# Kernel tuning notes

Hardware: AMD Instinct MI355X
Metric: run time of the kernel (lower is better)

Reference implementation:

```python
import jax, jax.numpy as jnp
import numpy as np
import math

HEAD_DIM = 64
N_Q = 64
N_KV = 8
HIDDEN = 2880
SLIDING = 128
BASE = 150000.0
INIT_CTX = 4096
SCALE = 32.0
NTK_A = 1.0
NTK_B = 32.0
SEQ = 2048


def _rope_cos_sin(position_ids):
    # YaRN-scaled inverse frequencies (scaling_factor > 1 branch)
    freq = BASE ** (jnp.arange(0, HEAD_DIM, 2, dtype=jnp.float32) / HEAD_DIM)
    concentration = 0.1 * math.log(SCALE) + 1.0
    d_half = HEAD_DIM // 2
    low = d_half * math.log(INIT_CTX / (NTK_B * 2 * math.pi)) / math.log(BASE)
    high = d_half * math.log(INIT_CTX / (NTK_A * 2 * math.pi)) / math.log(BASE)
    interpolation = 1.0 / (SCALE * freq)
    extrapolation = 1.0 / freq
    ramp = (jnp.arange(d_half, dtype=jnp.float32) - low) / (high - low)
    mask = 1.0 - jnp.clip(ramp, 0.0, 1.0)
    inv_freq = interpolation * (1.0 - mask) + extrapolation * mask
    freqs = position_ids.astype(jnp.float32)[:, None] * inv_freq[None, :]  # [n, d/2]
    return jnp.cos(freqs) * concentration, jnp.sin(freqs) * concentration


def _apply_rope(x, cos, sin):
    # x: [n, h, d]; cos/sin: [n, d/2]
    cos = cos[:, None, :].astype(x.dtype)
    sin = sin[:, None, :].astype(x.dtype)
    x1, x2 = jnp.split(x, 2, axis=-1)
    return jnp.concatenate([x1 * cos - x2 * sin, x2 * cos + x1 * sin], axis=-1)


def setup_inputs() -> dict:
    key = jax.random.key(0)
    ks = jax.random.split(key, 6)
    qkv_dim = HEAD_DIM * (N_Q + 2 * N_KV)
    return {
        "hidden_states": jax.random.normal(ks[0], (SEQ, HIDDEN), dtype=jnp.float32),
        "qkv_w": jax.random.normal(ks[1], (qkv_dim, HIDDEN), dtype=jnp.float32) * 0.02,
        "qkv_b": jax.random.normal(ks[2], (qkv_dim,), dtype=jnp.float32) * 0.02,
        "o_w": jax.random.normal(ks[3], (HIDDEN, N_Q * HEAD_DIM), dtype=jnp.float32) * 0.02,
        "o_b": jax.random.normal(ks[4], (HIDDEN,), dtype=jnp.float32) * 0.02,
        "sinks": jax.random.normal(ks[5], (N_Q,), dtype=jnp.float32),
        "position_ids": jnp.arange(SEQ, dtype=jnp.int64 if jax.config.jax_enable_x64 else jnp.int32),
    }


def reference(hidden_states, qkv_w, qkv_b, o_w, o_b, sinks, position_ids):
    n = hidden_states.shape[0]
    scaling = HEAD_DIM ** (-0.5)

    # fused QKV projection + split
    qkv = hidden_states @ qkv_w.T + qkv_b  # [n, (nq+2*nkv)*d]
    q_sz, k_sz = N_Q * HEAD_DIM, N_KV * HEAD_DIM
    q = qkv[:, :q_sz].reshape(n, N_Q, HEAD_DIM)
    k = qkv[:, q_sz:q_sz + k_sz].reshape(n, N_KV, HEAD_DIM)
    v = qkv[:, q_sz + k_sz:].reshape(n, N_KV, HEAD_DIM)

    # RoPE (YaRN)
    cos, sin = _rope_cos_sin(position_ids)
    q = _apply_rope(q, cos, sin)
    k = _apply_rope(k, cos, sin)

    # GQA: repeat KV heads to match query heads
    groups = N_Q // N_KV
    k_full = jnp.repeat(k, groups, axis=1)  # [n, N_Q, d]
    v_full = jnp.repeat(v, groups, axis=1)

    scores = jnp.einsum('qhd,khd->hqk', q, k_full) * scaling  # [H, S, S]

    # sliding-window mask (distance > window -> -inf), as in source (no causal term)
    current_pos = position_ids.max()
    key_pos = current_pos - n + 1 + jnp.arange(n)
    dist = position_ids[:, None] - key_pos[None, :]
    win_mask = jnp.where(dist > SLIDING, -jnp.inf, 0.0).astype(scores.dtype)
    scores = scores + win_mask[None, :, :]

    # learned sink logit appended to softmax normalization
    sink = jnp.broadcast_to(sinks[:, None, None], (N_Q, n, 1)).astype(scores.dtype)
    logits = jnp.concatenate([scores, sink], axis=-1)  # [H, S, S+1]
    probs = jax.nn.softmax(logits, axis=-1)[..., :-1]   # drop sink column

    attn = jnp.einsum('hqk,khd->qhd', probs, v_full)    # [S, H, d]
    attn = attn.reshape(n, N_Q * HEAD_DIM)
    return attn @ o_w.T + o_b
```

## Files before the change

kernel.cpp:

```cpp
#include <hip/hip_runtime.h>
#include <hip/hip_bf16.h>
#include <stdint.h>

typedef __attribute__((ext_vector_type(4))) float f32x4;
typedef __attribute__((ext_vector_type(8))) short bf16x8;

#define SEQ 2048
#define HIDDEN 2880
#define NQ 64
#define NKV 8
#define HD 64
#define QKV_DIM 5120
#define Q_SZ 4096
#define K_SZ 512
#define OW_N 2880
#define OW_NPAD 2944
#define OW_K 4096

__device__ __forceinline__ unsigned short f2b_bits(float f) {
    unsigned int x = __float_as_uint(f);
    unsigned int r = (x + 0x7fffu + ((x >> 16) & 1u)) >> 16;
    return (unsigned short)r;
}
__device__ __forceinline__ float b2f(unsigned short u) {
    return __uint_as_float(((unsigned int)u) << 16);
}

__device__ __forceinline__ void llds16(const ushort* g, ushort* l) {
    __builtin_amdgcn_global_load_lds(
        (const __attribute__((address_space(1))) void*)g,
        (__attribute__((address_space(3))) void*)l, 16, 0, 0);
}

__global__ void convert_all(const float* __restrict__ hidden, const float* __restrict__ qkv_w,
                            const float* __restrict__ o_w, ushort* __restrict__ hs_bf,
                            ushort* __restrict__ wqkv_bf, ushort* __restrict__ wo_bf) {
    const int N1 = SEQ * HIDDEN / 4;
    const int N2 = N1 + QKV_DIM * HIDDEN / 4;
    const int N3 = N2 + OW_NPAD * OW_K / 4;
    int i = blockIdx.x * blockDim.x + threadIdx.x;
    int stride = gridDim.x * blockDim.x;
    for (; i < N3; i += stride) {
        const float* src;
        ushort* dst;
        int j;
        if (i < N1) {
            j = i; src = hidden; dst = hs_bf;
        } else if (i < N2) {
            j = i - N1; src = qkv_w; dst = wqkv_bf;
        } else {
            j = i - N2; src = o_w; dst = wo_bf;
            if ((j >> 10) >= OW_N) {
                reinterpret_cast<ushort4*>(dst)[j] = make_ushort4(0, 0, 0, 0);
                continue;
            }
        }
        float4 v = reinterpret_cast<const float4*>(src)[j];
        reinterpret_cast<ushort4*>(dst)[j] =
            make_ushort4(f2b_bits(v.x), f2b_bits(v.y), f2b_bits(v.z), f2b_bits(v.w));
    }
}

template<int OUT_BF16>
__global__ __launch_bounds__(256) void gemm_bt(
    const ushort* __restrict__ A, const ushort* __restrict__ B,
    const float* __restrict__ bias, void* __restrict__ Cout,
    int M, int N, int K, int Nreal, int ldC)
{
    __shared__ __align__(16) ushort As[128 * 64];
    __shared__ __align__(16) ushort Bs[128 * 64];
    const int tid = threadIdx.x;
    const int lane = tid & 63;
    const int w = tid >> 6;
    const int wr = w >> 1, wc = w & 1;

    const int nwg = gridDim.x;
    const int per = nwg >> 3;
    const int wgid = (blockIdx.x & 7) * per + (blockIdx.x >> 3);
    const int m0 = (wgid & 15) * 128;
    const int n0 = (wgid >> 4) * 128;

    f32x4 acc[4][4] = {};

    for (int k0 = 0; k0 < K; k0 += 64) {
        #pragma unroll
        for (int it = 0; it < 4; ++it) {
            int i = it * 256 + tid;
            int row = i >> 3;
            int col16 = (i ^ (row & 7)) & 7;
            llds16(A + (size_t)(m0 + row) * K + k0 + col16 * 8,
                   As + (size_t)(it * 256 + (tid & ~63)) * 8);
            llds16(B + (size_t)(n0 + row) * K + k0 + col16 * 8,
                   Bs + (size_t)(it * 256 + (tid & ~63)) * 8);
        }
        __syncthreads();
        #pragma unroll
        for (int kk = 0; kk < 2; ++kk) {
            bf16x8 a[4], b[4];
            #pragma unroll
            for (int mi = 0; mi < 4; ++mi) {
                int row = wr * 64 + mi * 16 + (lane & 15);
                int byte = row * 128 + kk * 64 + (lane >> 4) * 16;
                byte ^= (row & 7) << 4;
                a[mi] = *reinterpret_cast<const bf16x8*>(reinterpret_cast<const char*>(As) + byte);
            }
            #pragma unroll
            for (int ni = 0; ni < 4; ++ni) {
                int row = wc * 64 + ni * 16 + (lane & 15);
                int byte = row * 128 + kk * 64 + (lane >> 4) * 16;
                byte ^= (row & 7) << 4;
                b[ni] = *reinterpret_cast<const bf16x8*>(reinterpret_cast<const char*>(Bs) + byte);
            }
            #pragma unroll
            for (int mi = 0; mi < 4; ++mi)
                #pragma unroll
                for (int ni = 0; ni < 4; ++ni)
                    acc[mi][ni] = __builtin_amdgcn_mfma_f32_16x16x32_bf16(a[mi], b[ni], acc[mi][ni], 0, 0, 0);
        }
        __syncthreads();
    }

    #pragma unroll
    for (int mi = 0; mi < 4; ++mi) {
        int gr = m0 + wr * 64 + mi * 16 + (lane >> 4) * 4;
        #pragma unroll
        for (int ni = 0; ni < 4; ++ni) {
            int gc = n0 + wc * 64 + ni * 16 + (lane & 15);
            if (gc < Nreal) {
                float bv = bias[gc];
                #pragma unroll
                for (int r = 0; r < 4; ++r) {
                    float v = acc[mi][ni][r] + bv;
                    if (OUT_BF16)
                        ((ushort*)Cout)[(size_t)(gr + r) * ldC + gc] = f2b_bits(v);
                    else
                        ((float*)Cout)[(size_t)(gr + r) * ldC + gc] = v;
                }
            }
        }
    }
}

template<int OUT_BF16>
__global__ __launch_bounds__(256) void gemm_bt64(
    const ushort* __restrict__ A, const ushort* __restrict__ B,
    const float* __restrict__ bias, void* __restrict__ Cout,
    int M, int N, int K, int Nreal, int ldC)
{
    __shared__ __align__(16) ushort As[64 * 64];
    __shared__ __align__(16) ushort Bs[128 * 64];
    const int tid = threadIdx.x;
    const int lane = tid & 63;
    const int w = tid >> 6;
    const int l15 = lane & 15;
    const int l4 = lane >> 4;

    const int nwg = gridDim.x;
    const int per = nwg >> 3;
    const int wgid = (blockIdx.x & 7) * per + (blockIdx.x >> 3);
    const int m0 = (wgid & 31) * 64;
    const int n0 = (wgid >> 5) * 128;

    f32x4 acc[4][2] = {};

    for (int k0 = 0; k0 < K; k0 += 64) {
        #pragma unroll
        for (int it = 0; it < 2; ++it) {
            int i = it * 256 + tid;
            int row = i >> 3;
            int col16 = (i ^ (row & 7)) & 7;
            llds16(A + (size_t)(m0 + row) * K + k0 + col16 * 8,
                   As + (size_t)(it * 256 + (tid & ~63)) * 8);
        }
        #pragma unroll
        for (int it = 0; it < 4; ++it) {
            int i = it * 256 + tid;
            int row = i >> 3;
            int col16 = (i ^ (row & 7)) & 7;
            llds16(B + (size_t)(n0 + row) * K + k0 + col16 * 8,
                   Bs + (size_t)(it * 256 + (tid & ~63)) * 8);
        }
        __syncthreads();
        #pragma unroll
        for (int kk = 0; kk < 2; ++kk) {
            bf16x8 a[4], b[2];
            #pragma unroll
            for (int mi = 0; mi < 4; ++mi) {
                int row = mi * 16 + l15;
                int byte = row * 128 + kk * 64 + l4 * 16;
                byte ^= (row & 7) << 4;
                a[mi] = *reinterpret_cast<const bf16x8*>(reinterpret_cast<const char*>(As) + byte);
            }
            #pragma unroll
            for (int ni = 0; ni < 2; ++ni) {
                int row = w * 32 + ni * 16 + l15;
                int byte = row * 128 + kk * 64 + l4 * 16;
                byte ^= (row & 7) << 4;
                b[ni] = *reinterpret_cast<const bf16x8*>(reinterpret_cast<const char*>(Bs) + byte);
            }
            #pragma unroll
            for (int mi = 0; mi < 4; ++mi)
                #pragma unroll
                for (int ni = 0; ni < 2; ++ni)
                    acc[mi][ni] = __builtin_amdgcn_mfma_f32_16x16x32_bf16(a[mi], b[ni], acc[mi][ni], 0, 0, 0);
        }
        __syncthreads();
    }

    #pragma unroll
    for (int mi = 0; mi < 4; ++mi) {
        int gr = m0 + mi * 16 + l4 * 4;
        #pragma unroll
        for (int ni = 0; ni < 2; ++ni) {
            int gc = n0 + w * 32 + ni * 16 + l15;
            if (gc < Nreal) {
                float bv = bias[gc];
                #pragma unroll
                for (int r = 0; r < 4; ++r) {
                    float v = acc[mi][ni][r] + bv;
                    if (OUT_BF16)
                        ((ushort*)Cout)[(size_t)(gr + r) * ldC + gc] = f2b_bits(v);
                    else
                        ((float*)Cout)[(size_t)(gr + r) * ldC + gc] = v;
                }
            }
        }
    }
}

__global__ __launch_bounds__(256) void rope_kernel(
    const ushort* __restrict__ qkv, const int* __restrict__ pos,
    ushort* __restrict__ q_ro, ushort* __restrict__ k_ro)
{
    __shared__ float cosv[32], sinv[32];
    const int s = blockIdx.x;
    const int tid = threadIdx.x;
    if (tid < 32) {
        int j = tid;
        const float logbase = logf(150000.0f);
        float freq = expf((float)j * (logbase / 32.0f));
        float interp = 1.0f / (32.0f * freq);
        float extrap = 1.0f / freq;
        const float twopi = 6.283185307179586f;
        float low  = 32.0f * logf(4096.0f / (32.0f * twopi)) / logbase;
        float high = 32.0f * logf(4096.0f / (1.0f  * twopi)) / logbase;
        float ramp = ((float)j - low) / (high - low);
        float mask = 1.0f - fminf(fmaxf(ramp, 0.0f), 1.0f);
        float inv_freq = interp * (1.0f - mask) + extrap * mask;
        float ang = (float)pos[s] * inv_freq;
        const float conc = 0.1f * logf(32.0f) + 1.0f;
        cosv[j] = cosf(ang) * conc;
        sinv[j] = sinf(ang) * conc;
    }
    __syncthreads();
    const float qsc = 0.125f * 1.4426950408889634f;
    #pragma unroll
    for (int it = 0; it < 8; ++it) {
        int idx = it * 256 + tid;
        int h = idx >> 5, j = idx & 31;
        const ushort* src = qkv + (size_t)s * QKV_DIM + h * HD;
        float x1 = b2f(src[j]), x2 = b2f(src[j + 32]);
        float c = cosv[j], sn = sinv[j];
        ushort* dst = q_ro + ((size_t)h * SEQ + s) * HD;
        dst[j]      = f2b_bits((x1 * c - x2 * sn) * qsc);
        dst[j + 32] = f2b_bits((x2 * c + x1 * sn) * qsc);
    }
    {
        int h = tid >> 5, j = tid & 31;
        const ushort* src = qkv + (size_t)s * QKV_DIM + Q_SZ + h * HD;
        float x1 = b2f(src[j]), x2 = b2f(src[j + 32]);
        float c = cosv[j], sn = sinv[j];
        ushort* dst = k_ro + ((size_t)h * SEQ + s) * HD;
        dst[j]      = f2b_bits(x1 * c - x2 * sn);
        dst[j + 32] = f2b_bits(x2 * c + x1 * sn);
    }
}

__global__ __launch_bounds__(256) void vtrans_kernel(const ushort* __restrict__ qkv, ushort* __restrict__ vT) {
    __shared__ ushort t[64][65];
    const int kh = blockIdx.x >> 5;
    const int s0 = (blockIdx.x & 31) * 64;
    const int tid = threadIdx.x;
    #pragma unroll
    for (int it = 0; it < 16; ++it) {
        int e = it * 256 + tid;
        int sl = e >> 6, d = e & 63;
        t[d][sl] = qkv[(size_t)(s0 + sl) * QKV_DIM + Q_SZ + K_SZ + kh * HD + d];
    }
    __syncthreads();
    #pragma unroll
    for (int it = 0; it < 16; ++it) {
        int e = it * 256 + tid;
        int d = e >> 6, sl = e & 63;
        vT[((size_t)kh * HD + d) * SEQ + s0 + sl] = t[d][sl];
    }
}

__global__ __launch_bounds__(256, 4) void attn_kernel(
    const ushort* __restrict__ q_ro, const ushort* __restrict__ k_ro,
    const ushort* __restrict__ vT, const float* __restrict__ sinks,
    ushort* __restrict__ attn_out)
{
    __shared__ __align__(16) ushort Kb[2][4096];
    __shared__ __align__(16) ushort Vb[2][4096];

    const int tid = threadIdx.x;
    const int lane = tid & 63;
    const int w = tid >> 6;
    const int l15 = lane & 15;
    const int l4 = lane >> 4;

    int wg = blockIdx.x;
    int wgid = (wg & 7) * 128 + (wg >> 3);
    const int kh = wgid >> 7;
    const int qh = (wgid >> 4) & 7;
    const int pp = wgid & 15;
    const int h = kh * 8 + qh;

    const float snk = sinks[h];

    const short oneb = (short)0x3F80;
    const bf16x8 bones = {oneb, oneb, oneb, oneb, oneb, oneb, oneb, oneb};

    const int i0 = tid, i1 = 256 + tid;
    const int r0 = i0 >> 3, cs0 = (i0 ^ r0) & 7;
    const int r1 = i1 >> 3, cs1 = (i1 ^ r1) & 7;
    const ushort* gK0 = k_ro + (size_t)kh * (SEQ * 64) + r0 * 64 + cs0 * 8;
    const ushort* gK1 = k_ro + (size_t)kh * (SEQ * 64) + r1 * 64 + cs1 * 8;
    const ushort* gV0 = vT + ((size_t)kh * 64 + r0) * SEQ + cs0 * 8;
    const ushort* gV1 = vT + ((size_t)kh * 64 + r1) * SEQ + cs1 * 8;
    const int ld0 = (tid & ~63) * 8, ld1 = (256 + (tid & ~63)) * 8;

    const int swz = (l15 & 7) << 4;
    const int kvbase = l15 * 128 + ((l4 * 16) ^ swz);
    const int pwbase = l15 * 128 + ((l4 * 8) ^ swz);

    auto stage = [&](int bs, int k0) {
        llds16(gK0 + k0 * 64, &Kb[bs][ld0]);
        llds16(gK1 + k0 * 64, &Kb[bs][ld1]);
        llds16(gV0 + k0,      &Vb[bs][ld0]);
        llds16(gV1 + k0,      &Vb[bs][ld1]);
    };

    for (int sidx = 0; sidx < 2; ++sidx) {
        const int qt = sidx ? (31 - pp) : pp;
        const int q0 = qt * 64;
        const int qw = q0 + w * 16;

        bf16x8 aq[2];
        #pragma unroll
        for (int kc = 0; kc < 2; ++kc)
            aq[kc] = *reinterpret_cast<const bf16x8*>(
                q_ro + ((size_t)h * SEQ + qw + l15) * HD + kc * 32 + l4 * 8);

        f32x4 o[4] = {};
        f32x4 lacc = {0.f, 0.f, 0.f, 0.f};

        const int kt0 = (qt >= 2) ? (qt - 2) : 0;
        int cur = 0;

        stage(0, kt0 * 64);
        __syncthreads();

        for (int kt = kt0; kt < SEQ / 64; ++kt) {
            const int k0 = kt * 64;
            if (kt + 1 < SEQ / 64) stage(cur ^ 1, k0 + 64);

            f32x4 s[4];
            const f32x4 z = {0.f, 0.f, 0.f, 0.f};
            const char* kbp = (const char*)Kb[cur];
            __builtin_amdgcn_s_setprio(1);
            #pragma unroll
            for (int c = 0; c < 4; ++c) {
                bf16x8 bk0 = *reinterpret_cast<const bf16x8*>(kbp + c * 2048 + kvbase);
                s[c] = __builtin_amdgcn_mfma_f32_16x16x32_bf16(bk0, aq[0], z, 0, 0, 0);
                bf16x8 bk1 = *reinterpret_cast<const bf16x8*>(kbp + c * 2048 + (kvbase ^ 64));
                s[c] = __builtin_amdgcn_mfma_f32_16x16x32_bf16(bk1, aq[1], s[c], 0, 0, 0);
            }
            __builtin_amdgcn_s_setprio(0);

            if (k0 < qw - 113) {
                int thr = qw + l15 - 128 - k0;
                #pragma unroll
                for (int c = 0; c < 4; ++c)
                    #pragma unroll
                    for (int r = 0; r < 4; ++r)
                        if (c * 16 + l4 * 4 + r < thr) s[c][r] = -1e30f;
            }

            __builtin_amdgcn_s_barrier();
            char* pw = (char*)Kb[cur] + w * 2048;

            #pragma unroll
            for (int c = 0; c < 4; ++c) {
                float p0 = exp2f(s[c][0]), p1 = exp2f(s[c][1]);
                float p2 = exp2f(s[c][2]), p3 = exp2f(s[c][3]);
                unsigned int pk0, pk1;
                asm("v_cvt_pk_bf16_f32 %0, %1, %2" : "=v"(pk0) : "v"(p0), "v"(p1));
                asm("v_cvt_pk_bf16_f32 %0, %1, %2" : "=v"(pk1) : "v"(p2), "v"(p3));
                uint2 pv; pv.x = pk0; pv.y = pk1;
                *reinterpret_cast<uint2*>(pw + (pwbase ^ (c * 32))) = pv;
            }

            const char* vbp = (const char*)Vb[cur];
            __builtin_amdgcn_s_setprio(1);
            #pragma unroll
            for (int kc = 0; kc < 2; ++kc) {
                bf16x8 pa = *reinterpret_cast<const bf16x8*>(pw + (kvbase ^ (kc * 64)));
                lacc = __builtin_amdgcn_mfma_f32_16x16x32_bf16(pa, bones, lacc, 0, 0, 0);
                #pragma unroll
                for (int df = 0; df < 4; ++df) {
                    bf16x8 bv = *reinterpret_cast<const bf16x8*>(vbp + df * 2048 + (kvbase ^ (kc * 64)));
                    o[df] = __builtin_amdgcn_mfma_f32_16x16x32_bf16(pa, bv, o[df], 0, 0, 0);
                }
            }
            __builtin_amdgcn_s_setprio(0);

            __syncthreads();
            cur ^= 1;
        }

        {
            const float es = exp2f(snk * 1.4426950408889634f);
            float inv[4];
            #pragma unroll
            for (int r = 0; r < 4; ++r) inv[r] = 1.0f / (lacc[r] + es);
            #pragma unroll
            for (int df = 0; df < 4; ++df)
                #pragma unroll
                for (int r = 0; r < 4; ++r) {
                    int row = qw + l4 * 4 + r;
                    int col = df * 16 + l15;
                    attn_out[(size_t)row * Q_SZ + h * HD + col] = f2b_bits(o[df][r] * inv[r]);
                }
        }
    }
}

extern "C" void kernel_launch(void* const* d_in, const int* in_sizes, int n_in,
                              void* d_out, int out_size, void* d_ws, size_t ws_size,
                              hipStream_t stream) {
    const float* hidden = (const float*)d_in[0];
    const float* qkv_w  = (const float*)d_in[1];
    const float* qkv_b  = (const float*)d_in[2];
    const float* o_w    = (const float*)d_in[3];
    const float* o_b    = (const float*)d_in[4];
    const float* sinks  = (const float*)d_in[5];
    const int*   pos    = (const int*)d_in[6];
    float* out = (float*)d_out;

    char* ws = (char*)d_ws;
    size_t off = 0;
    auto alloc = [&](size_t bytes) {
        char* p = ws + off;
        off += (bytes + 255) & ~(size_t)255;
        return p;
    };
    ushort* hs_bf   = (ushort*)alloc((size_t)SEQ * HIDDEN * 2);
    ushort* wqkv_bf = (ushort*)alloc((size_t)QKV_DIM * HIDDEN * 2);
    ushort* qkv_bf  = (ushort*)alloc((size_t)SEQ * QKV_DIM * 2);
    ushort* q_ro    = (ushort*)alloc((size_t)NQ * SEQ * HD * 2);
    ushort* k_ro    = (ushort*)alloc((size_t)NKV * SEQ * HD * 2);
    ushort* vT      = (ushort*)alloc((size_t)NKV * HD * SEQ * 2);
    ushort* attn_bf = (ushort*)alloc((size_t)SEQ * Q_SZ * 2);
    ushort* wo_bf   = (ushort*)alloc((size_t)OW_NPAD * OW_K * 2);

    convert_all<<<2048, 256, 0, stream>>>(hidden, qkv_w, o_w, hs_bf, wqkv_bf, wo_bf);

    gemm_bt<1><<<(QKV_DIM / 128) * (SEQ / 128), 256, 0, stream>>>(
        hs_bf, wqkv_bf, qkv_b, qkv_bf, SEQ, QKV_DIM, HIDDEN, QKV_DIM, QKV_DIM);

    rope_kernel<<<SEQ, 256, 0, stream>>>(qkv_bf, pos, q_ro, k_ro);
    vtrans_kernel<<<NKV * 32, 256, 0, stream>>>(qkv_bf, vT);

    attn_kernel<<<1024, 256, 0, stream>>>(q_ro, k_ro, vT, sinks, attn_bf);

    gemm_bt64<0><<<(OW_NPAD / 128) * (SEQ / 64), 256, 0, stream>>>(
        attn_bf, wo_bf, o_b, out, SEQ, OW_NPAD, OW_K, OW_N, OW_N);
}
```

Baseline: 262.0 us.

## Process both query strips in one KV sweep with a dedicated P buffer

Each workgroup used to handle its two query tiles (pp and 31-pp) one after the other, loading the K/V stream twice. Now a single pass over the KV tiles serves both, so strip B reuses the already staged K/V tiles once its window starts. The probability tile moves from the K buffer into a separate per-wave LDS array, which removes the extra barrier before the P write. The cost is more accumulator registers (two sets of o, lacc and q fragments) and more LDS per block, which may lower occupancy at launch bounds of 4.

```diff
diff --git a/kernel.cpp b/kernel.cpp
--- a/kernel.cpp
+++ b/kernel.cpp
@@ -303,6 +303,7 @@
 {
     __shared__ __align__(16) ushort Kb[2][4096];
     __shared__ __align__(16) ushort Vb[2][4096];
+    __shared__ __align__(16) ushort Pl[4][1024];
 
     const int tid = threadIdx.x;
     const int lane = tid & 63;
@@ -318,6 +319,7 @@
     const int h = kh * 8 + qh;
 
     const float snk = sinks[h];
+    char* pbase = (char*)&Pl[w][0];
 
     const short oneb = (short)0x3F80;
     const bf16x8 bones = {oneb, oneb, oneb, oneb, oneb, oneb, oneb, oneb};
@@ -342,98 +344,108 @@
         llds16(gV1 + k0,      &Vb[bs][ld1]);
     };
 
-    for (int sidx = 0; sidx < 2; ++sidx) {
-        const int qt = sidx ? (31 - pp) : pp;
-        const int q0 = qt * 64;
-        const int qw = q0 + w * 16;
-
-        bf16x8 aq[2];
-        #pragma unroll
-        for (int kc = 0; kc < 2; ++kc)
-            aq[kc] = *reinterpret_cast<const bf16x8*>(
-                q_ro + ((size_t)h * SEQ + qw + l15) * HD + kc * 32 + l4 * 8);
-
-        f32x4 o[4] = {};
-        f32x4 lacc = {0.f, 0.f, 0.f, 0.f};
-
-        const int kt0 = (qt >= 2) ? (qt - 2) : 0;
-        int cur = 0;
-
-        stage(0, kt0 * 64);
+    const int qtA = pp;
+    const int qtB = 31 - pp;
+    const int qwA = qtA * 64 + w * 16;
+    const int qwB = qtB * 64 + w * 16;
+    const int ktA0 = (qtA >= 2) ? (qtA - 2) : 0;
+    const int ktB0 = qtB - 2;
+
+    bf16x8 aqA[2], aqB[2];
+    #pragma unroll
+    for (int kc = 0; kc < 2; ++kc) {
+        aqA[kc] = *reinterpret_cast<const bf16x8*>(
+            q_ro + ((size_t)h * SEQ + qwA + l15) * HD + kc * 32 + l4 * 8);
+        aqB[kc] = *reinterpret_cast<const bf16x8*>(
+            q_ro + ((size_t)h * SEQ + qwB + l15) * HD + kc * 32 + l4 * 8);
+    }
+
+    f32x4 oA[4] = {}, oB[4] = {};
+    f32x4 laccA = {0.f, 0.f, 0.f, 0.f}, laccB = {0.f, 0.f, 0.f, 0.f};
+
+    int cur = 0;
+    stage(0, ktA0 * 64);
+    __syncthreads();
+
+    auto strip_body = [&](const bf16x8 (&aq)[2], f32x4 (&o)[4], f32x4& lacc,
+                          int qw, int k0, const char* kbp, const char* vbp) {
+        f32x4 s[4];
+        const f32x4 z = {0.f, 0.f, 0.f, 0.f};
+        __builtin_amdgcn_s_setprio(1);
+        #pragma unroll
+        for (int c = 0; c < 4; ++c) {
+            bf16x8 bk0 = *reinterpret_cast<const bf16x8*>(kbp + c * 2048 + kvbase);
+            s[c] = __builtin_amdgcn_mfma_f32_16x16x32_bf16(bk0, aq[0], z, 0, 0, 0);
+            bf16x8 bk1 = *reinterpret_cast<const bf16x8*>(kbp + c * 2048 + (kvbase ^ 64));
+            s[c] = __builtin_amdgcn_mfma_f32_16x16x32_bf16(bk1, aq[1], s[c], 0, 0, 0);
+        }
+        __builtin_amdgcn_s_setprio(0);
+
+        if (k0 < qw - 113) {
+            int thr = qw + l15 - 128 - k0;
+            #pragma unroll
+            for (int c = 0; c < 4; ++c)
+                #pragma unroll
+                for (int r = 0; r < 4; ++r)
+                    if (c * 16 + l4 * 4 + r < thr) s[c][r] = -1e30f;
+        }
+
+        #pragma unroll
+        for (int c = 0; c < 4; ++c) {
+            float p0 = exp2f(s[c][0]), p1 = exp2f(s[c][1]);
+            float p2 = exp2f(s[c][2]), p3 = exp2f(s[c][3]);
+            unsigned int pk0, pk1;
+            asm("v_cvt_pk_bf16_f32 %0, %1, %2" : "=v"(pk0) : "v"(p0), "v"(p1));
+            asm("v_cvt_pk_bf16_f32 %0, %1, %2" : "=v"(pk1) : "v"(p2), "v"(p3));
+            uint2 pv; pv.x = pk0; pv.y = pk1;
+            *reinterpret_cast<uint2*>(pbase + (pwbase ^ (c * 32))) = pv;
+        }
+
+        __builtin_amdgcn_s_setprio(1);
+        #pragma unroll
+        for (int kc = 0; kc < 2; ++kc) {
+            bf16x8 pa = *reinterpret_cast<const bf16x8*>(pbase + (kvbase ^ (kc * 64)));
+            lacc = __builtin_amdgcn_mfma_f32_16x16x32_bf16(pa, bones, lacc, 0, 0, 0);
+            #pragma unroll
+            for (int df = 0; df < 4; ++df) {
+                bf16x8 bv = *reinterpret_cast<const bf16x8*>(vbp + df * 2048 + (kvbase ^ (kc * 64)));
+                o[df] = __builtin_amdgcn_mfma_f32_16x16x32_bf16(pa, bv, o[df], 0, 0, 0);
+            }
+        }
+        __builtin_amdgcn_s_setprio(0);
+    };
+
+    for (int kt = ktA0; kt < SEQ / 64; ++kt) {
+        const int k0 = kt * 64;
+        if (kt + 1 < SEQ / 64) stage(cur ^ 1, k0 + 64);
+
+        const char* kbp = (const char*)Kb[cur];
+        const char* vbp = (const char*)Vb[cur];
+        strip_body(aqA, oA, laccA, qwA, k0, kbp, vbp);
+        if (kt >= ktB0) strip_body(aqB, oB, laccB, qwB, k0, kbp, vbp);
+
         __syncthreads();
-
-        for (int kt = kt0; kt < SEQ / 64; ++kt) {
-            const int k0 = kt * 64;
-            if (kt + 1 < SEQ / 64) stage(cur ^ 1, k0 + 64);
-
-            f32x4 s[4];
-            const f32x4 z = {0.f, 0.f, 0.f, 0.f};
-            const char* kbp = (const char*)Kb[cur];
-            __builtin_amdgcn_s_setprio(1);
-            #pragma unroll
-            for (int c = 0; c < 4; ++c) {
-                bf16x8 bk0 = *reinterpret_cast<const bf16x8*>(kbp + c * 2048 + kvbase);
-                s[c] = __builtin_amdgcn_mfma_f32_16x16x32_bf16(bk0, aq[0], z, 0, 0, 0);
-                bf16x8 bk1 = *reinterpret_cast<const bf16x8*>(kbp + c * 2048 + (kvbase ^ 64));
-                s[c] = __builtin_amdgcn_mfma_f32_16x16x32_bf16(bk1, aq[1], s[c], 0, 0, 0);
-            }
-            __builtin_amdgcn_s_setprio(0);
-
-            if (k0 < qw - 113) {
-                int thr = qw + l15 - 128 - k0;
-                #pragma unroll
-                for (int c = 0; c < 4; ++c)
-                    #pragma unroll
-                    for (int r = 0; r < 4; ++r)
-                        if (c * 16 + l4 * 4 + r < thr) s[c][r] = -1e30f;
-            }
-
-            __builtin_amdgcn_s_barrier();
-            char* pw = (char*)Kb[cur] + w * 2048;
-
-            #pragma unroll
-            for (int c = 0; c < 4; ++c) {
-                float p0 = exp2f(s[c][0]), p1 = exp2f(s[c][1]);
-                float p2 = exp2f(s[c][2]), p3 = exp2f(s[c][3]);
-                unsigned int pk0, pk1;
-                asm("v_cvt_pk_bf16_f32 %0, %1, %2" : "=v"(pk0) : "v"(p0), "v"(p1));
-                asm("v_cvt_pk_bf16_f32 %0, %1, %2" : "=v"(pk1) : "v"(p2), "v"(p3));
-                uint2 pv; pv.x = pk0; pv.y = pk1;
-                *reinterpret_cast<uint2*>(pw + (pwbase ^ (c * 32))) = pv;
-            }
-
-            const char* vbp = (const char*)Vb[cur];
-            __builtin_amdgcn_s_setprio(1);
-            #pragma unroll
-            for (int kc = 0; kc < 2; ++kc) {
-                bf16x8 pa = *reinterpret_cast<const bf16x8*>(pw + (kvbase ^ (kc * 64)));
-                lacc = __builtin_amdgcn_mfma_f32_16x16x32_bf16(pa, bones, lacc, 0, 0, 0);
-                #pragma unroll
-                for (int df = 0; df < 4; ++df) {
-                    bf16x8 bv = *reinterpret_cast<const bf16x8*>(vbp + df * 2048 + (kvbase ^ (kc * 64)));
-                    o[df] = __builtin_amdgcn_mfma_f32_16x16x32_bf16(pa, bv, o[df], 0, 0, 0);
-                }
-            }
-            __builtin_amdgcn_s_setprio(0);
-
-            __syncthreads();
-            cur ^= 1;
-        }
-
-        {
-            const float es = exp2f(snk * 1.4426950408889634f);
-            float inv[4];
-            #pragma unroll
-            for (int r = 0; r < 4; ++r) inv[r] = 1.0f / (lacc[r] + es);
-            #pragma unroll
-            for (int df = 0; df < 4; ++df)
-                #pragma unroll
-                for (int r = 0; r < 4; ++r) {
-                    int row = qw + l4 * 4 + r;
-                    int col = df * 16 + l15;
-                    attn_out[(size_t)row * Q_SZ + h * HD + col] = f2b_bits(o[df][r] * inv[r]);
-                }
-        }
+        cur ^= 1;
+    }
+
+    {
+        const float es = exp2f(snk * 1.4426950408889634f);
+        float invA[4], invB[4];
+        #pragma unroll
+        for (int r = 0; r < 4; ++r) {
+            invA[r] = 1.0f / (laccA[r] + es);
+            invB[r] = 1.0f / (laccB[r] + es);
+        }
+        #pragma unroll
+        for (int df = 0; df < 4; ++df)
+            #pragma unroll
+            for (int r = 0; r < 4; ++r) {
+                int col = df * 16 + l15;
+                int rowA = qwA + l4 * 4 + r;
+                attn_out[(size_t)rowA * Q_SZ + h * HD + col] = f2b_bits(oA[df][r] * invA[r]);
+                int rowB = qwB + l4 * 4 + r;
+                attn_out[(size_t)rowB * Q_SZ + h * HD + col] = f2b_bits(oB[df][r] * invB[r]);
+            }
     }
 }
 
```

After: 255.8 us, median of 3. 1.02x faster.
